# Kernel tuning notes

Hardware: AMD Instinct MI355X
Metric: run time of the kernel (lower is better)

The kernel has to match this reference:

```python
import jax, jax.numpy as jnp
import numpy as np

B, H, Wd, CIN = 4, 64, 64, 65   # batch, height, width, in_channels (incl. time)
COUT = 256                      # out_channels (incl. time)
K = 3
KK = K * K
PAD, STRIDE = 1, 1
SOUT = 4                        # output_stabilizer_size (C4 rotations)
CURV = 1.0                      # Lorentz manifold curvature k
LIN_FEAT = (CIN - 1) * KK + 1   # 577


def make_c4_z2_indices(ksize):
    # (out_rotation, in_stabilizer=1, u, v, [s, u_src, v_src]) index table,
    # realizing the C4 filter rotation as a gather (as in GrouPy).
    f = np.arange(ksize * ksize).reshape(ksize, ksize)
    inds = np.zeros((4, 1, ksize, ksize, 3), dtype=np.int64)
    for r in range(4):
        rot = np.rot90(f, r)
        u, v = np.unravel_index(rot, (ksize, ksize))
        inds[r, 0, :, :, 1] = u
        inds[r, 0, :, :, 2] = v
    return inds

INDS = make_c4_z2_indices(K)


def setup_inputs() -> dict:
    key = jax.random.key(0)
    k1, k2, k3 = jax.random.split(key, 3)
    stdv = float(np.sqrt(2.0 / ((CIN - 1) * KK)))  # reset_parameters
    x = jax.random.normal(k1, (B, H, Wd, CIN), dtype=jnp.float32)
    W = jax.random.uniform(k2, (COUT, LIN_FEAT), minval=-stdv, maxval=stdv, dtype=jnp.float32)
    b = jax.random.uniform(k3, (COUT,), minval=-stdv, maxval=stdv, dtype=jnp.float32)
    return {"x": x, "W": W, "b": b}


def _unfold(x):
    # x: (B, C, H, W) -> (B, C*KK, Ho*Wo) in torch.nn.Unfold layout (channel-major, kernel-minor)
    xp = jnp.pad(x, ((0, 0), (0, 0), (PAD, PAD), (PAD, PAD)))
    ho = (H + 2 * PAD - K) // STRIDE + 1
    wo = (Wd + 2 * PAD - K) // STRIDE + 1
    cols = [xp[:, :, i:i + ho * STRIDE:STRIDE, j:j + wo * STRIDE:STRIDE]
            for i in range(K) for j in range(K)]
    p = jnp.stack(cols, axis=2)  # (B, C, KK, ho, wo)
    return p.reshape(B, CIN * KK, ho * wo), ho, wo


def _forward(x, W, b):
    # torch code does x.view(B, C, H, W) on channel-last data: a reshape, not a permute.
    xv = x.reshape(B, CIN, H, Wd)
    patches, ho, wo = _unfold(xv)
    patches = jnp.transpose(patches, (0, 2, 1))          # (B, P, C*KK)
    P = patches.shape[1]
    patches = patches.reshape(B, P, CIN, 1, K, K)
    patches = jnp.broadcast_to(patches, (B, P, CIN, SOUT, K, K))  # repeat over group dim
    # --- group-equivariant filter transform realized as a gather on patches ---
    ir = INDS.reshape(-1, 3)                              # (SOUT*KK, 3)
    pi = patches[:, :, :, ir[:, 0], ir[:, 1], ir[:, 2]]   # (B, P, C, SOUT*KK)
    pi = pi.reshape(B, P, CIN, SOUT, KK)
    pt = jnp.transpose(pi, (3, 0, 1, 2, 4)).reshape(SOUT, B, P, CIN * KK)
    # --- extract_lorentz_patches (vectorized over group dim) ---
    sqrt_k = jnp.sqrt(jnp.float32(CURV))
    t = jnp.maximum(pt[..., :KK], sqrt_k)                 # clamp time components
    t_resc = jnp.sqrt(jnp.sum(t * t, axis=-1, keepdims=True) - (KK - 1) * CURV)
    sp = pt[..., KK:]                                     # (SOUT,B,P,(C-1)*KK) channel-major
    sp = sp.reshape(SOUT, B, P, CIN - 1, KK).swapaxes(-1, -2).reshape(SOUT, B, P, (CIN - 1) * KK)
    pre = jnp.concatenate([t_resc, sp], axis=-1)          # (SOUT,B,P,LIN_FEAT)
    # --- LorentzFullyConnected: linear, then recompute time from space norm ---
    y = jnp.einsum('gbpf,of->gbpo', pre, W) + b           # (SOUT,B,P,COUT)
    y_sp = y[..., 1:]
    y_t = jnp.sqrt(jnp.sum(y_sp * y_sp, axis=-1, keepdims=True) + CURV)
    out = jnp.concatenate([y_t, y_sp], axis=-1)
    out = jnp.transpose(out, (1, 0, 2, 3)).reshape(B, SOUT, ho, wo, COUT)
    return out


def reference(x, W, b):
    return _forward(x, W, b)
```

## Files before the change

### kernel.cpp

```cpp
#include <hip/hip_runtime.h>
#include <hip/hip_bf16.h>

#define CIN 65
#define LIN 577
#define NSTEP 18
#define M_  16384

typedef __bf16 bf16x8 __attribute__((ext_vector_type(8)));
typedef float  f32x4  __attribute__((ext_vector_type(4)));
typedef unsigned short u16x8 __attribute__((ext_vector_type(8)));

__constant__ int SIG[4][9] = {
  {0,1,2,3,4,5,6,7,8},
  {2,5,8,1,4,7,0,3,6},
  {8,7,6,5,4,3,2,1,0},
  {6,3,0,7,4,1,8,5,2}};

__device__ __forceinline__ int swzm(int r) { return (r ^ (r >> 2)) & 3; }

__global__ __launch_bounds__(512) void prep_k(const float* __restrict__ x,
                                              const float* __restrict__ W,
                                              __hip_bfloat16* __restrict__ A,
                                              __hip_bfloat16* __restrict__ Wg,
                                              float* __restrict__ T) {
  __shared__ float lds[CIN * 3 * 72];
  const int tid = threadIdx.x;
  if (blockIdx.x >= 256) {
    int pidx = (blockIdx.x - 256) * 512 + tid;
    int jc  = pidx & 3;
    int col = (pidx >> 2) & 255;
    int t   = pidx >> 10;
    int ks  = t % NSTEP, g = t / NSTEP;
    int k   = SIG[(4 - g) & 3][ks >> 1];
    const float* src = W + col * LIN + 1 + k * 64 + (ks & 1) * 32 + jc * 8;
    u16x8 pk;
#pragma unroll
    for (int e = 0; e < 8; ++e) {
      union { __hip_bfloat16 h; unsigned short u; } cv;
      cv.h = __float2bfloat16(src[e]);
      pk[e] = cv.u;
    }
    *(u16x8*)(Wg + (size_t)pidx * 8) = pk;
    return;
  }
  const int b = blockIdx.x >> 6, py = blockIdx.x & 63;
  const float* xb = x + (size_t)b * (CIN * 4096);
  for (int i = tid; i < CIN * 3 * 18; i += 512)
    *(f32x4*)&lds[i * 4] = (f32x4){0.f, 0.f, 0.f, 0.f};
  __syncthreads();
  for (int i = tid; i < CIN * 3 * 16; i += 512) {
    int pr = i >> 4, j = i & 15;
    int c = pr / 3, dy = pr - c * 3;
    int hy = py + dy - 1;
    if (hy >= 0 && hy < 64)
      *(f32x4*)&lds[c * 216 + dy * 72 + 4 + j * 4] =
          *(const f32x4*)(xb + c * 4096 + hy * 64 + j * 4);
  }
  __syncthreads();

  const int wave = tid >> 6, px = tid & 63;
  const int rowid = (blockIdx.x << 6) | px;
#pragma unroll
  for (int qi = 0; qi < 9; ++qi) {
    int q = wave * 9 + qi;
    int m = q >> 3, cb8 = q & 7;
    int dy = m / 3, dx = m - dy * 3;
    const float* src = &lds[(1 + cb8 * 8) * 216 + dy * 72 + 3 + dx + px];
    u16x8 pk;
#pragma unroll
    for (int e = 0; e < 8; ++e) {
      union { __hip_bfloat16 h; unsigned short u; } cv;
      cv.h = __float2bfloat16(src[e * 216]);
      pk[e] = cv.u;
    }
    *(u16x8*)(A + ((size_t)q * M_ + rowid) * 8) = pk;
  }
  if (wave == 0) {
    float s = 0.f;
#pragma unroll
    for (int m = 0; m < 9; ++m) {
      float t = fmaxf(lds[(m / 3) * 72 + 3 + (m % 3) + px], 1.f);
      s += t * t;
    }
    T[rowid] = sqrtf(s - 8.f);
  }
}

__device__ __forceinline__ void async_cp16(const void* g, void* ldsbase) {
  __builtin_amdgcn_global_load_lds(
      (const __attribute__((address_space(1))) void*)g,
      (__attribute__((address_space(3))) void*)ldsbase, 16, 0, 0);
}

__global__ __launch_bounds__(512, 4) void gemm_k(const __hip_bfloat16* __restrict__ A,
                                                 const __hip_bfloat16* __restrict__ Wg,
                                                 const float* __restrict__ W,
                                                 const float* __restrict__ bias,
                                                 const float* __restrict__ T,
                                                 float* __restrict__ out) {
  __shared__ __align__(16) char smem[49152];
  const int fid = blockIdx.x;
  const int lid = ((fid & 7) << 6) | (fid >> 3);
  const int g = lid & 3, rb = lid >> 2;
  const int brow = rb << 7;
  const int tid = threadIdx.x, wave = tid >> 6, lane = tid & 63;
  const int fr = lane & 15, fq = lane >> 4;
  const int wr = (wave >> 2) * 64, wcb = (wave & 3) * 64;

  const int arow = tid >> 2;
  const int alc  = (tid & 3) ^ swzm(arow);
  const int bcol0 = tid >> 2;
  const int blc0  = (tid & 3) ^ swzm(bcol0);
  const int bcol1 = 128 + (tid >> 2);
  const int blc1  = (tid & 3) ^ swzm(bcol1);
  f32x4 acc[4][4] = {};

  auto STAGE = [&](int buf, int ks) {
    int qb = (ks >> 1) * 8 + (ks & 1) * 4;
    async_cp16(A + (((size_t)(qb + alc) * M_ + brow + arow) << 3),
               smem + buf * 8192 + wave * 1024);
    const __hip_bfloat16* bs = Wg + ((size_t)(g * NSTEP + ks) << 13);
    char* bl = smem + 16384 + buf * 16384 + wave * 1024;
    async_cp16(bs + bcol0 * 32 + blc0 * 8, bl);
    async_cp16(bs + bcol1 * 32 + blc1 * 8, bl + 8192);
  };
  auto COMPUTE = [&](int buf) {
    const char* Ab = smem + buf * 8192;
    const char* Bb = smem + 16384 + buf * 16384;
    bf16x8 af[4], bf[4];
#pragma unroll
    for (int i = 0; i < 4; ++i) {
      int r = wr + i * 16 + fr;
      af[i] = *(const bf16x8*)(Ab + r * 64 + ((fq ^ swzm(r)) << 4));
    }
#pragma unroll
    for (int j = 0; j < 4; ++j) {
      int c = wcb + j * 16 + fr;
      bf[j] = *(const bf16x8*)(Bb + c * 64 + ((fq ^ swzm(c)) << 4));
    }
#pragma unroll
    for (int i = 0; i < 4; ++i)
#pragma unroll
      for (int j = 0; j < 4; ++j)
        acc[i][j] = __builtin_amdgcn_mfma_f32_16x16x32_bf16(af[i], bf[j], acc[i][j], 0, 0, 0);
  };

  STAGE(0, 0);
  __syncthreads();
  int cur = 0;
  for (int ks = 0; ks < NSTEP - 1; ++ks) {
    STAGE(cur ^ 1, ks + 1);
    COMPUTE(cur);
    __syncthreads();
    cur ^= 1;
  }
  float* Tsh = (float*)smem;
  float* Ps  = (float*)(smem + 512);
  if (tid < 128) Tsh[tid] = T[brow + tid];
  COMPUTE(cur);
  __syncthreads();

  float bo[4], w0v[4]; int oc[4];
#pragma unroll
  for (int j = 0; j < 4; ++j) {
    oc[j]  = wcb + j * 16 + fr;
    bo[j]  = bias[oc[j]];
    w0v[j] = W[oc[j] * LIN];
  }
#pragma unroll
  for (int i = 0; i < 4; ++i) {
#pragma unroll
    for (int rr = 0; rr < 4; ++rr) {
      int rl = wr + i * 16 + fq * 4 + rr;
      int row = brow + rl;
      size_t obase = ((size_t)(((row >> 12) * 4 + g) * 4096 + (row & 4095)) << 8);
      float tval = Tsh[rl];
      float s = 0.f;
#pragma unroll
      for (int j = 0; j < 4; ++j) {
        float y = acc[i][j][rr] + bo[j] + tval * w0v[j];
        if (oc[j] != 0) { s += y * y; out[obase + oc[j]] = y; }
      }
      s += __shfl_xor(s, 1); s += __shfl_xor(s, 2);
      s += __shfl_xor(s, 4); s += __shfl_xor(s, 8);
      if (fr == 0) Ps[rl * 4 + (wave & 3)] = s;
    }
  }
  __syncthreads();
  if (tid < 128) {
    int row = brow + tid;
    float s = Ps[tid * 4] + Ps[tid * 4 + 1] + Ps[tid * 4 + 2] + Ps[tid * 4 + 3] + 1.0f;
    out[(size_t)(((row >> 12) * 4 + g) * 4096 + (row & 4095)) << 8] = sqrtf(s);
  }
}

extern "C" void kernel_launch(void* const* d_in, const int* in_sizes, int n_in,
                              void* d_out, int out_size, void* d_ws, size_t ws_size,
                              hipStream_t stream) {
  const float* x    = (const float*)d_in[0];
  const float* W    = (const float*)d_in[1];
  const float* bias = (const float*)d_in[2];
  float* out = (float*)d_out;

  char* ws = (char*)d_ws;
  __hip_bfloat16* Wg = (__hip_bfloat16*)ws;
  float*          T  = (float*)(ws + 1179648);
  __hip_bfloat16* A  = (__hip_bfloat16*)(ws + 1245184);

  prep_k<<<400, 512, 0, stream>>>(x, W, A, Wg, T);
  gemm_k<<<512, 512, 0, stream>>>(A, Wg, W, bias, T, out);
}
```

Measured before the change: 44.53 us.

## Triple-buffer GEMM LDS stages with explicit vmcnt waits and MFMA priority

Moves the GEMM main loop from double to triple buffering in LDS. Two stages are issued ahead, and each iteration waits with an explicit s_waitcnt vmcnt on only the oldest stage's async copies, then uses a single barrier instead of a sync after every compute. It also raises wave priority around the MFMA block with s_setprio. The cost is 72KB of LDS per block instead of 48KB, which may limit how many blocks fit per CU. The hand-written vmcnt counts and buffer-rotation bookkeeping are a correctness risk.

```diff
diff --git a/kernel.cpp b/kernel.cpp
--- a/kernel.cpp
+++ b/kernel.cpp
@@ -98,7 +98,7 @@
                                                  const float* __restrict__ bias,
                                                  const float* __restrict__ T,
                                                  float* __restrict__ out) {
-  __shared__ __align__(16) char smem[49152];
+  __shared__ __align__(16) char smem[73728];
   const int fid = blockIdx.x;
   const int lid = ((fid & 7) << 6) | (fid >> 3);
   const int g = lid & 3, rb = lid >> 2;
@@ -115,18 +115,14 @@
   const int blc1  = (tid & 3) ^ swzm(bcol1);
   f32x4 acc[4][4] = {};
 
-  auto STAGE = [&](int buf, int ks) {
+  auto STAGE = [&](char* pa, char* pb, int ks) {
     int qb = (ks >> 1) * 8 + (ks & 1) * 4;
-    async_cp16(A + (((size_t)(qb + alc) * M_ + brow + arow) << 3),
-               smem + buf * 8192 + wave * 1024);
+    async_cp16(A + (((size_t)(qb + alc) * M_ + brow + arow) << 3), pa + wave * 1024);
     const __hip_bfloat16* bs = Wg + ((size_t)(g * NSTEP + ks) << 13);
-    char* bl = smem + 16384 + buf * 16384 + wave * 1024;
-    async_cp16(bs + bcol0 * 32 + blc0 * 8, bl);
-    async_cp16(bs + bcol1 * 32 + blc1 * 8, bl + 8192);
+    async_cp16(bs + bcol0 * 32 + blc0 * 8, pb + wave * 1024);
+    async_cp16(bs + bcol1 * 32 + blc1 * 8, pb + wave * 1024 + 8192);
   };
-  auto COMPUTE = [&](int buf) {
-    const char* Ab = smem + buf * 8192;
-    const char* Bb = smem + 16384 + buf * 16384;
+  auto COMPUTE = [&](const char* Ab, const char* Bb) {
     bf16x8 af[4], bf[4];
 #pragma unroll
     for (int i = 0; i < 4; ++i) {
@@ -138,28 +134,36 @@
       int c = wcb + j * 16 + fr;
       bf[j] = *(const bf16x8*)(Bb + c * 64 + ((fq ^ swzm(c)) << 4));
     }
+    __builtin_amdgcn_s_setprio(1);
 #pragma unroll
     for (int i = 0; i < 4; ++i)
 #pragma unroll
       for (int j = 0; j < 4; ++j)
         acc[i][j] = __builtin_amdgcn_mfma_f32_16x16x32_bf16(af[i], bf[j], acc[i][j], 0, 0, 0);
+    __builtin_amdgcn_s_setprio(0);
   };
 
-  STAGE(0, 0);
-  __syncthreads();
-  int cur = 0;
-  for (int ks = 0; ks < NSTEP - 1; ++ks) {
-    STAGE(cur ^ 1, ks + 1);
-    COMPUTE(cur);
-    __syncthreads();
-    cur ^= 1;
-  }
   float* Tsh = (float*)smem;
-  float* Ps  = (float*)(smem + 512);
-  if (tid < 128) Tsh[tid] = T[brow + tid];
-  COMPUTE(cur);
-  __syncthreads();
-
+  char *cA = smem,         *nA = smem + 8192,  *tA = smem + 16384;
+  char *cB = smem + 24576, *nB = smem + 40960, *tB = smem + 57344;
+  STAGE(cA, cB, 0);
+  STAGE(nA, nB, 1);
+  for (int ks = 0; ks < NSTEP; ++ks) {
+    if (ks < NSTEP - 1) {
+      asm volatile("s_waitcnt vmcnt(3)" ::: "memory");
+    } else {
+      asm volatile("s_waitcnt vmcnt(0)" ::: "memory");
+    }
+    __builtin_amdgcn_s_barrier();
+    if (ks + 2 < NSTEP) STAGE(tA, tB, ks + 2);
+    if (ks == NSTEP - 1 && tid < 128) Tsh[tid] = T[brow + tid];
+    COMPUTE(cA, cB);
+    char* r = cA; cA = nA; nA = tA; tA = r;
+    r = cB; cB = nB; nB = tB; tB = r;
+  }
+  __syncthreads();
+
+  float* Ps = (float*)(smem + 512);
   float bo[4], w0v[4]; int oc[4];
 #pragma unroll
   for (int j = 0; j < 4; ++j) {
```

Result: faster. 43.48 us (-2.4%).

## Halve GEMM row tile to 64 and double grid for more occupancy

Applied to the files above, without the earlier changes.

The GEMM block tile drops from 128 to 64 rows (8 waves now each own 32x64), and the grid grows from 512 to 1024 blocks with the swizzle and launch bounds adjusted to allow more resident blocks. Shared memory shrinks and the T load moves to the kernel start, which also removes the separate final compute step. The MFMA section is wrapped in setprio so math gets priority over loads. The cost is that each B (weight) tile is now reused over fewer rows, so weight traffic per output roughly doubles, and half the threads sit idle during A staging.

```diff
diff --git a/kernel.cpp b/kernel.cpp
--- a/kernel.cpp
+++ b/kernel.cpp
@@ -92,44 +92,48 @@
       (__attribute__((address_space(3))) void*)ldsbase, 16, 0, 0);
 }
 
-__global__ __launch_bounds__(512, 4) void gemm_k(const __hip_bfloat16* __restrict__ A,
+__global__ __launch_bounds__(512, 6) void gemm_k(const __hip_bfloat16* __restrict__ A,
                                                  const __hip_bfloat16* __restrict__ Wg,
                                                  const float* __restrict__ W,
                                                  const float* __restrict__ bias,
                                                  const float* __restrict__ T,
                                                  float* __restrict__ out) {
-  __shared__ __align__(16) char smem[49152];
+  __shared__ __align__(16) char smem[42240];
   const int fid = blockIdx.x;
-  const int lid = ((fid & 7) << 6) | (fid >> 3);
+  const int lid = ((fid & 7) << 7) | (fid >> 3);
   const int g = lid & 3, rb = lid >> 2;
-  const int brow = rb << 7;
+  const int brow = rb << 6;
   const int tid = threadIdx.x, wave = tid >> 6, lane = tid & 63;
   const int fr = lane & 15, fq = lane >> 4;
-  const int wr = (wave >> 2) * 64, wcb = (wave & 3) * 64;
+  const int wr = (wave >> 2) * 32, wcb = (wave & 3) * 64;
+
+  float* Tsh = (float*)(smem + 40960);
+  float* Ps  = (float*)(smem + 41216);
+  if (tid < 64) Tsh[tid] = T[brow + tid];
 
   const int arow = tid >> 2;
   const int alc  = (tid & 3) ^ swzm(arow);
-  const int bcol0 = tid >> 2;
-  const int blc0  = (tid & 3) ^ swzm(bcol0);
-  const int bcol1 = 128 + (tid >> 2);
-  const int blc1  = (tid & 3) ^ swzm(bcol1);
-  f32x4 acc[4][4] = {};
+  const int bc0  = tid >> 2, bl0 = (tid & 3) ^ swzm(bc0);
+  const int bc1  = 128 + (tid >> 2), bl1 = (tid & 3) ^ swzm(bc1);
+  const __hip_bfloat16* Wgg = Wg + ((size_t)(g * NSTEP) << 13);
 
   auto STAGE = [&](int buf, int ks) {
-    int qb = (ks >> 1) * 8 + (ks & 1) * 4;
-    async_cp16(A + (((size_t)(qb + alc) * M_ + brow + arow) << 3),
-               smem + buf * 8192 + wave * 1024);
-    const __hip_bfloat16* bs = Wg + ((size_t)(g * NSTEP + ks) << 13);
-    char* bl = smem + 16384 + buf * 16384 + wave * 1024;
-    async_cp16(bs + bcol0 * 32 + blc0 * 8, bl);
-    async_cp16(bs + bcol1 * 32 + blc1 * 8, bl + 8192);
+    if (tid < 256)
+      async_cp16(A + (((size_t)(ks * 4 + alc) * M_ + brow + arow) << 3),
+                 smem + buf * 4096 + wave * 1024);
+    const __hip_bfloat16* bs = Wgg + ((size_t)ks << 13);
+    char* bl = smem + 8192 + buf * 16384 + wave * 1024;
+    async_cp16(bs + bc0 * 32 + bl0 * 8, bl);
+    async_cp16(bs + bc1 * 32 + bl1 * 8, bl + 8192);
   };
+
+  f32x4 acc[2][4] = {};
   auto COMPUTE = [&](int buf) {
-    const char* Ab = smem + buf * 8192;
-    const char* Bb = smem + 16384 + buf * 16384;
-    bf16x8 af[4], bf[4];
-#pragma unroll
-    for (int i = 0; i < 4; ++i) {
+    const char* Ab = smem + buf * 4096;
+    const char* Bb = smem + 8192 + buf * 16384;
+    bf16x8 af[2], bf[4];
+#pragma unroll
+    for (int i = 0; i < 2; ++i) {
       int r = wr + i * 16 + fr;
       af[i] = *(const bf16x8*)(Ab + r * 64 + ((fq ^ swzm(r)) << 4));
     }
@@ -138,27 +142,22 @@
       int c = wcb + j * 16 + fr;
       bf[j] = *(const bf16x8*)(Bb + c * 64 + ((fq ^ swzm(c)) << 4));
     }
-#pragma unroll
-    for (int i = 0; i < 4; ++i)
+    __builtin_amdgcn_s_setprio(1);
+#pragma unroll
+    for (int i = 0; i < 2; ++i)
 #pragma unroll
       for (int j = 0; j < 4; ++j)
         acc[i][j] = __builtin_amdgcn_mfma_f32_16x16x32_bf16(af[i], bf[j], acc[i][j], 0, 0, 0);
+    __builtin_amdgcn_s_setprio(0);
   };
 
   STAGE(0, 0);
   __syncthreads();
-  int cur = 0;
-  for (int ks = 0; ks < NSTEP - 1; ++ks) {
-    STAGE(cur ^ 1, ks + 1);
-    COMPUTE(cur);
+  for (int ks = 0; ks < NSTEP; ++ks) {
+    if (ks + 1 < NSTEP) STAGE((ks + 1) & 1, ks + 1);
+    COMPUTE(ks & 1);
     __syncthreads();
-    cur ^= 1;
-  }
-  float* Tsh = (float*)smem;
-  float* Ps  = (float*)(smem + 512);
-  if (tid < 128) Tsh[tid] = T[brow + tid];
-  COMPUTE(cur);
-  __syncthreads();
+  }
 
   float bo[4], w0v[4]; int oc[4];
 #pragma unroll
@@ -168,7 +167,7 @@
     w0v[j] = W[oc[j] * LIN];
   }
 #pragma unroll
-  for (int i = 0; i < 4; ++i) {
+  for (int i = 0; i < 2; ++i) {
 #pragma unroll
     for (int rr = 0; rr < 4; ++rr) {
       int rl = wr + i * 16 + fq * 4 + rr;
@@ -187,7 +186,7 @@
     }
   }
   __syncthreads();
-  if (tid < 128) {
+  if (tid < 64) {
     int row = brow + tid;
     float s = Ps[tid * 4] + Ps[tid * 4 + 1] + Ps[tid * 4 + 2] + Ps[tid * 4 + 3] + 1.0f;
     out[(size_t)(((row >> 12) * 4 + g) * 4096 + (row & 4095)) << 8] = sqrtf(s);
@@ -208,5 +207,5 @@
   __hip_bfloat16* A  = (__hip_bfloat16*)(ws + 1245184);
 
   prep_k<<<400, 512, 0, stream>>>(x, W, A, Wg, T);
-  gemm_k<<<512, 512, 0, stream>>>(A, Wg, W, bias, T, out);
-}
+  gemm_k<<<1024, 512, 0, stream>>>(A, Wg, W, bias, T, out);
+}
```

Result: slower. 50.10 us (+12.5%).
